# Optimization experiments

Hardware: AMD Instinct MI355X
Metric: run time of the kernel (lower is better)

## Reference

```python
import jax, jax.numpy as jnp
import numpy as np

S, B, D, H, F = 2048, 4, 1024, 2, 2048
HD = D // H  # head dim = 512
EPS = 1e-8   # forward() hardcodes 1e-8, ignoring init eps


def rmsnorm(x, w):
    ms = jnp.mean(x * x, axis=-1, keepdims=True)
    return w * (x / jnp.sqrt(ms + EPS))


def setup_inputs() -> dict:
    key = jax.random.key(0)
    ks = jax.random.split(key, 12)
    s = 0.02
    return {
        "x": jax.random.normal(ks[0], (S, B, D), jnp.float32),
        "w_norm1": 1.0 + s * jax.random.normal(ks[1], (D,), jnp.float32),
        "in_proj_w": s * jax.random.normal(ks[2], (3 * D, D), jnp.float32),
        "in_proj_b": s * jax.random.normal(ks[3], (3 * D,), jnp.float32),
        "out_proj_w": s * jax.random.normal(ks[4], (D, D), jnp.float32),
        "out_proj_b": s * jax.random.normal(ks[5], (D,), jnp.float32),
        "w_norm2": 1.0 + s * jax.random.normal(ks[6], (D,), jnp.float32),
        "W1": s * jax.random.normal(ks[7], (F, D), jnp.float32),
        "b1": s * jax.random.normal(ks[8], (F,), jnp.float32),
        "W2": s * jax.random.normal(ks[9], (D, F), jnp.float32),
        "b2": s * jax.random.normal(ks[10], (D,), jnp.float32),
    }


def reference(x, w_norm1, in_proj_w, in_proj_b, out_proj_w, out_proj_b,
              w_norm2, W1, b1, W2, b2):
    # pre-norm
    h = rmsnorm(x, w_norm1)                      # (S,B,D)
    # packed qkv projection (torch MultiheadAttention in_proj)
    qkv = h @ in_proj_w.T + in_proj_b            # (S,B,3D)
    q, k, v = jnp.split(qkv, 3, axis=-1)
    # (S,B,D) -> (B,H,S,HD)
    def heads(t):
        return t.reshape(S, B, H, HD).transpose(1, 2, 0, 3)
    q, k, v = heads(q), heads(k), heads(v)
    scores = jnp.einsum("bhsd,bhtd->bhst", q, k) / jnp.sqrt(jnp.float32(HD))
    causal = jnp.tril(jnp.ones((S, S), bool))
    scores = jnp.where(causal, scores, -jnp.inf)
    attn = jax.nn.softmax(scores, axis=-1)       # (B,H,S,S)
    ctx = jnp.einsum("bhst,bhtd->bhsd", attn, v)  # (B,H,S,HD)
    ctx = ctx.transpose(2, 0, 1, 3).reshape(S, B, D)
    attn_out = ctx @ out_proj_w.T + out_proj_b
    # residual 1
    x1 = x + attn_out
    # MLP: Linear -> exact GELU -> Linear
    m = rmsnorm(x1, w_norm2)
    mlp = jax.nn.gelu(m @ W1.T + b1, approximate=False) @ W2.T + b2
    return x1 + mlp
```

## Files before the change

### kernel.cpp

```cpp
#include <hip/hip_runtime.h>


typedef __bf16 bf16;
typedef bf16 bf16x8 __attribute__((ext_vector_type(8)));
typedef bf16 bf16x4 __attribute__((ext_vector_type(4)));
typedef float f32x4 __attribute__((ext_vector_type(4)));

#define MFMA16x16x32(A, B, C) __builtin_amdgcn_mfma_f32_16x16x32_bf16(A, B, C, 0, 0, 0)

__device__ __forceinline__ void gload16(const void* g, void* l) {
  __builtin_amdgcn_global_load_lds(
      (const __attribute__((address_space(1))) void*)g,
      (__attribute__((address_space(3))) void*)l, 16, 0, 0);
}

__global__ __launch_bounds__(256) void wcvt4(
    const float* __restrict__ s0, bf16* __restrict__ d0,
    const float* __restrict__ s1, bf16* __restrict__ d1,
    const float* __restrict__ s2, bf16* __restrict__ d2,
    const float* __restrict__ s3, bf16* __restrict__ d3)
{
  const int gid = blockIdx.x * 256 + threadIdx.x;
  const float* s; bf16* d; int off;
  if (gid < 786432)       { s = s0; d = d0; off = gid; }
  else if (gid < 1048576) { s = s1; d = d1; off = gid - 786432; }
  else if (gid < 1572864) { s = s2; d = d2; off = gid - 1048576; }
  else                    { s = s3; d = d3; off = gid - 1572864; }
  const int i = off * 4;
  const float4 v = *(const float4*)(s + i);
  bf16x4 o;
  o[0] = (bf16)v.x; o[1] = (bf16)v.y; o[2] = (bf16)v.z; o[3] = (bf16)v.w;
  *(bf16x4*)(d + i) = o;
}

__global__ __launch_bounds__(256) void rmsnorm_kernel(
    const float* __restrict__ x, const float* __restrict__ w, bf16* __restrict__ out)
{
  const int row = blockIdx.x;
  const int tid = threadIdx.x;
  const float4 v = *(const float4*)(x + (size_t)row * 1024 + tid * 4);
  float ss = v.x * v.x + v.y * v.y + v.z * v.z + v.w * v.w;
#pragma unroll
  for (int off = 1; off < 64; off <<= 1) ss += __shfl_xor(ss, off, 64);
  __shared__ float red[4];
  if ((tid & 63) == 0) red[tid >> 6] = ss;
  __syncthreads();
  const float tot = red[0] + red[1] + red[2] + red[3];
  const float inv = rsqrtf(tot * (1.0f / 1024.0f) + 1e-8f);
  const float4 g = *(const float4*)(w + tid * 4);
  bf16x4 o;
  o[0] = (bf16)(v.x * g.x * inv);
  o[1] = (bf16)(v.y * g.y * inv);
  o[2] = (bf16)(v.z * g.z * inv);
  o[3] = (bf16)(v.w * g.w * inv);
  *(bf16x4*)(out + (size_t)row * 1024 + tid * 4) = o;
}

enum { EPI_BF16 = 0, EPI_RES = 1, EPI_GELU = 2, EPI_QKV = 3 };

template <int EPI>
__global__ __launch_bounds__(256, 3) void gemm_bt2(
    const bf16* __restrict__ A,
    const bf16* __restrict__ B,
    const float* __restrict__ bias,
    const float* res,
    float* outF, bf16* outQ, bf16* outK, bf16* outV,
    int M, int N, int K)
{
  __shared__ bf16 lds[3 * 8192];
  const int tid = threadIdx.x;
  const int Nb = N >> 7;
  const int lin = blockIdx.x;
  const int sup = lin / (Nb << 4);
  const int rem = lin - sup * (Nb << 4);
  const int bm = (sup << 4) + (rem & 15);
  const int bn = rem >> 4;
  const int w = tid >> 6, lane = tid & 63;
  const int q = lane >> 4, lr = lane & 15;
  const int wr = (w >> 1) * 64, wc = (w & 1) * 64;
  f32x4 acc[4][4] = {};
  const int srow = lane >> 2;
  const int gch = ((lane & 3) - ((lane >> 3) & 3)) & 3;
  const bf16* Ab = A + (size_t)(bm * 128) * K;
  const bf16* Bb = B + (size_t)(bn * 128) * K;
  const int sw = ((q + (lr >> 1)) & 3) * 16;
  const int NK = K >> 5;

#define STAGE(dst, k0)                                                        \
  {                                                                           \
    bf16* De = (dst);                                                         \
    _Pragma("unroll")                                                         \
    for (int c = 0; c < 2; c++) {                                             \
      const int r = (w * 2 + c) * 16 + srow;                                  \
      gload16(Ab + (size_t)r * K + (k0) + gch * 8, De + (w * 2 + c) * 512);   \
      gload16(Bb + (size_t)r * K + (k0) + gch * 8, De + 4096 + (w * 2 + c) * 512); \
    }                                                                         \
  }

  bf16* rd = &lds[0];
  bf16* nx = &lds[8192];
  bf16* st = &lds[16384];
  STAGE(rd, 0);
  STAGE(nx, 32);
  asm volatile("s_waitcnt vmcnt(2)" ::: "memory");
  __builtin_amdgcn_s_barrier();
  asm volatile("" ::: "memory");

#pragma unroll 1
  for (int u = 0; u < NK; ++u) {
    if (u + 2 < NK) STAGE(st, (u + 2) * 32);
    const char* As = (const char*)rd;
    const char* Bs = (const char*)(rd + 4096);
    bf16x8 af[4], bfr[4];
#pragma unroll
    for (int mt = 0; mt < 4; mt++)
      af[mt] = *(const bf16x8*)(As + (wr + mt * 16 + lr) * 64 + sw);
#pragma unroll
    for (int nt = 0; nt < 4; nt++)
      bfr[nt] = *(const bf16x8*)(Bs + (wc + nt * 16 + lr) * 64 + sw);
#pragma unroll
    for (int mt = 0; mt < 4; mt++)
#pragma unroll
      for (int nt = 0; nt < 4; nt++)
        acc[mt][nt] = MFMA16x16x32(af[mt], bfr[nt], acc[mt][nt]);
    if (u + 1 < NK) {
      if (u + 2 < NK)
        asm volatile("s_waitcnt vmcnt(2) lgkmcnt(0)" ::: "memory");
      else
        asm volatile("s_waitcnt vmcnt(0) lgkmcnt(0)" ::: "memory");
      __builtin_amdgcn_s_barrier();
      asm volatile("" ::: "memory");
    }
    bf16* t = rd; rd = nx; nx = st; st = t;
  }
#undef STAGE

  const int gm0 = bm * 128 + wr + q * 4;
  const int gn0 = bn * 128 + wc + lr;
  bf16* outs = nullptr;
  if constexpr (EPI == EPI_QKV) {
    const int reg = (bn * 128) >> 10;
    outs = reg == 0 ? outQ : (reg == 1 ? outK : outV);
  } else {
    outs = outQ;
  }
#pragma unroll
  for (int nt = 0; nt < 4; nt++) {
    const int gn = gn0 + nt * 16;
    const float bv = bias[gn];
#pragma unroll
    for (int mt = 0; mt < 4; mt++) {
#pragma unroll
      for (int r = 0; r < 4; r++) {
        float v = acc[mt][nt][r] + bv;
        const int gm = gm0 + mt * 16 + r;
        if constexpr (EPI == EPI_GELU) {
          v = 0.5f * v * (1.0f + erff(v * 0.70710678118654752f));
          outs[(size_t)gm * N + gn] = (bf16)v;
        } else if constexpr (EPI == EPI_BF16) {
          outs[(size_t)gm * N + gn] = (bf16)v;
        } else if constexpr (EPI == EPI_QKV) {
          outs[(size_t)gm * 1024 + (gn & 1023)] = (bf16)v;
        } else {
          const size_t idx = (size_t)gm * N + gn;
          outF[idx] = v + res[idx];
        }
      }
    }
  }
}

__global__ __launch_bounds__(256) void vtrans_kernel(
    const bf16* __restrict__ vtmp, bf16* __restrict__ vt)
{
  __shared__ bf16 tile[64 * 72];
  const int kt = blockIdx.x;
  const int dt = blockIdx.y;
  const int bh = blockIdx.z;
  const int b = bh >> 1, h = bh & 1;
  const int tid = threadIdx.x;
#pragma unroll
  for (int it = 0; it < 2; it++) {
    const int key = it * 32 + (tid >> 3);
    const int dc = (tid & 7) * 8;
    const bf16x8 v = *(const bf16x8*)(vtmp +
        (size_t)((kt * 64 + key) * 4 + b) * 1024 + h * 512 + dt * 64 + dc);
    *(bf16x8*)&tile[key * 72 + dc] = v;
  }
  __syncthreads();
#pragma unroll
  for (int it = 0; it < 2; it++) {
    const int dim = it * 32 + (tid >> 3);
    const int kc = (tid & 7) * 8;
    bf16x8 o;
#pragma unroll
    for (int j = 0; j < 8; j++) o[j] = tile[(kc + j) * 72 + dim];
    *(bf16x8*)(vt + (size_t)bh * (1u << 20) +
               (size_t)(dt * 64 + dim) * 2048 + kt * 64 + kc) = o;
  }
}

__global__ __launch_bounds__(768, 3) void attn_kernel(
    const bf16* __restrict__ qb, const bf16* __restrict__ kb,
    const bf16* __restrict__ vtg, bf16* __restrict__ opart,
    float* __restrict__ lpart)
{
  __shared__ bf16 Ks[2][32 * 520];
  __shared__ bf16 Ps[2][4][16 * 40];
  const int bh = blockIdx.x;
  const int y = blockIdx.y;
  const int b = bh >> 1, h = bh & 1;
  const int tid = threadIdx.x;
  const int w = tid >> 6, lane = tid & 63;
  const int q = lane >> 4, lr = lane & 15;
  const float sc = 0.044194173824159216f;

  if (w < 4) {
    const bf16* krow0 = kb + (size_t)b * 1024 + h * 512 + lane * 8;
    for (int piece = 0; piece < 2; ++piece) {
      const int qt = piece ? (31 - y) : y;
      const int qrow0 = qt * 64;
      const int c0 = piece ? (qt + 1) : 0;
      const int c1 = c0 + qt + 1;
      bf16x8 Qf[16];
      {
        const bf16* qp = qb + (size_t)((qrow0 + w * 16 + lr) * 4 + b) * 1024 + h * 512 + q * 8;
#pragma unroll
        for (int kk = 0; kk < 16; kk++) Qf[kk] = *(const bf16x8*)(qp + kk * 32);
      }
#pragma unroll
      for (int j = 0; j < 8; j++)
        gload16(krow0 + (size_t)((c0 * 32 + w * 8 + j) * 4) * 1024,
                &Ks[c0 & 1][(w * 8 + j) * 520]);
      __syncthreads();
      const int myrow = qrow0 + w * 16 + q * 4;
      for (int t = c0; t <= c1; t++) {
        if (t < c1) {
          const int p = t & 1;
          const int kc = t * 32;
          if (t + 1 < c1) {
            const int kc2 = (t + 1) * 32;
#pragma unroll
            for (int j = 0; j < 8; j++)
              gload16(krow0 + (size_t)((kc2 + w * 8 + j) * 4) * 1024,
                      &Ks[1 - p][(w * 8 + j) * 520]);
          }
          const bool dead = kc > qrow0 + w * 16 + 15;
          float p0[4], p1[4];
          if (!dead) {
            f32x4 S0 = {}, S1 = {};
#pragma unroll
            for (int kk = 0; kk < 16; kk++) {
              const bf16x8 k0 = *(const bf16x8*)&Ks[p][lr * 520 + kk * 32 + q * 8];
              const bf16x8 k1 = *(const bf16x8*)&Ks[p][(16 + lr) * 520 + kk * 32 + q * 8];
              S0 = MFMA16x16x32(Qf[kk], k0, S0);
              S1 = MFMA16x16x32(Qf[kk], k1, S1);
            }
#pragma unroll
            for (int r = 0; r < 4; r++) {
              const int row = myrow + r;
              p0[r] = (kc + lr > row) ? 0.f : __expf(S0[r] * sc);
              p1[r] = (kc + 16 + lr > row) ? 0.f : __expf(S1[r] * sc);
            }
          } else {
#pragma unroll
            for (int r = 0; r < 4; r++) { p0[r] = 0.f; p1[r] = 0.f; }
          }
#pragma unroll
          for (int r = 0; r < 4; r++) {
            Ps[p][w][(q * 4 + r) * 40 + lr] = (bf16)p0[r];
            Ps[p][w][(q * 4 + r) * 40 + 16 + lr] = (bf16)p1[r];
          }
        }
        __syncthreads();
      }
    }
  } else {
    const int pw = w - 4;
    bf16x8 ones;
#pragma unroll
    for (int e = 0; e < 8; e++) ones[e] = (bf16)1.0f;
    const bf16* vbase = vtg + ((size_t)bh << 20) + (size_t)(pw * 64 + lr) * 2048 + q * 8;
    for (int piece = 0; piece < 2; ++piece) {
      const int qt = piece ? (31 - y) : y;
      const int qrow0 = qt * 64;
      const int c0 = piece ? (qt + 1) : 0;
      const int c1 = c0 + qt + 1;
      f32x4 O[4][4] = {};
      f32x4 lac = {};
      __syncthreads();
      for (int t = c0; t <= c1; t++) {
        if (t > c0) {
          const int p = (t - 1) & 1;
          const int kc = (t - 1) * 32;
          bf16x8 pa[4];
#pragma unroll
          for (int rt = 0; rt < 4; rt++)
            pa[rt] = *(const bf16x8*)&Ps[p][rt][lr * 40 + q * 8];
          if (pw < 4) {
            const bf16x8 psel = pw == 0 ? pa[0] : (pw == 1 ? pa[1] : (pw == 2 ? pa[2] : pa[3]));
            lac = MFMA16x16x32(psel, ones, lac);
          }
#pragma unroll
          for (int ct = 0; ct < 4; ct++) {
            const bf16x8 vf = *(const bf16x8*)(vbase + (size_t)(ct * 16) * 2048 + kc);
#pragma unroll
            for (int rt = 0; rt < 4; rt++)
              O[rt][ct] = MFMA16x16x32(pa[rt], vf, O[rt][ct]);
          }
        }
        __syncthreads();
      }
      bf16* op = opart + (size_t)piece * (8u << 20) + (size_t)bh * (1u << 20);
#pragma unroll
      for (int rt = 0; rt < 4; rt++)
#pragma unroll
        for (int ct = 0; ct < 4; ct++)
#pragma unroll
          for (int r = 0; r < 4; r++)
            op[(size_t)(qrow0 + rt * 16 + q * 4 + r) * 512 + pw * 64 + ct * 16 + lr] =
                (bf16)O[rt][ct][r];
      if (lr == 0 && pw < 4) {
#pragma unroll
        for (int r = 0; r < 4; r++)
          lpart[piece * 16384 + bh * 2048 + qrow0 + pw * 16 + q * 4 + r] = lac[r];
      }
    }
  }
}

__global__ __launch_bounds__(256) void attn_combine(
    const bf16* __restrict__ opart, const float* __restrict__ lpart,
    bf16* __restrict__ ctx)
{
  const int gid = blockIdx.x * 256 + threadIdx.x;
  const int bh = gid >> 17;
  const int rem = gid & 131071;
  const int row = rem >> 6;
  const int dc = (rem & 63) * 8;
  const size_t o = (size_t)bh * (1u << 20) + (size_t)row * 512 + dc;
  const bf16x8 a = *(const bf16x8*)(opart + o);
  const bf16x8 c = *(const bf16x8*)(opart + (size_t)(8u << 20) + o);
  const float inv = 1.0f /
      (lpart[bh * 2048 + row] + lpart[16384 + bh * 2048 + row]);
  bf16x8 ov;
#pragma unroll
  for (int e = 0; e < 8; e++) ov[e] = (bf16)(((float)a[e] + (float)c[e]) * inv);
  const int b = bh >> 1, h = bh & 1;
  *(bf16x8*)(ctx + (size_t)(row * 4 + b) * 1024 + h * 512 + dc) = ov;
}

extern "C" void kernel_launch(void* const* d_in, const int* in_sizes, int n_in,
                              void* d_out, int out_size, void* d_ws, size_t ws_size,
                              hipStream_t stream)
{
  (void)in_sizes; (void)n_in; (void)out_size; (void)ws_size;
  const float* x    = (const float*)d_in[0];
  const float* wn1  = (const float*)d_in[1];
  const float* wqkv = (const float*)d_in[2];
  const float* bqkv = (const float*)d_in[3];
  const float* wout = (const float*)d_in[4];
  const float* bout = (const float*)d_in[5];
  const float* wn2  = (const float*)d_in[6];
  const float* W1   = (const float*)d_in[7];
  const float* b1   = (const float*)d_in[8];
  const float* W2   = (const float*)d_in[9];
  const float* b2   = (const float*)d_in[10];
  float* out = (float*)d_out;

  char* ws = (char*)d_ws;
  const size_t Mi = 1u << 20;
  bf16* S0v = (bf16*)(ws);
  bf16* S1v = (bf16*)(ws + 16 * Mi);
  bf16* S2v = (bf16*)(ws + 32 * Mi);
  bf16* S3v = (bf16*)(ws + 48 * Mi);
  bf16* wqb = (bf16*)(ws + 64 * Mi);
  bf16* wob = (bf16*)(ws + 70 * Mi);
  bf16* w1b = (bf16*)(ws + 72 * Mi);
  bf16* w2b = (bf16*)(ws + 76 * Mi);
  const int M = 8192;

  wcvt4<<<8192, 256, 0, stream>>>(wqkv, wqb, wout, wob, W1, w1b, W2, w2b);
  rmsnorm_kernel<<<8192, 256, 0, stream>>>(x, wn1, S0v);
  gemm_bt2<EPI_QKV><<<64 * 24, 256, 0, stream>>>(
      S0v, wqb, bqkv, nullptr, nullptr, S1v, S2v, S3v, M, 3072, 1024);
  vtrans_kernel<<<dim3(32, 8, 8), 256, 0, stream>>>(S3v, S0v);
  attn_kernel<<<dim3(8, 32), 768, 0, stream>>>(
      S1v, S2v, S0v, (bf16*)d_out, (float*)S3v);
  attn_combine<<<4096, 256, 0, stream>>>((const bf16*)d_out, (const float*)S3v, S1v);
  gemm_bt2<EPI_RES><<<64 * 8, 256, 0, stream>>>(
      S1v, wob, bout, x, out, nullptr, nullptr, nullptr, M, 1024, 1024);
  rmsnorm_kernel<<<8192, 256, 0, stream>>>(out, wn2, S0v);
  gemm_bt2<EPI_GELU><<<64 * 16, 256, 0, stream>>>(
      S0v, w1b, b1, nullptr, nullptr, S2v, nullptr, nullptr, M, 2048, 1024);
  gemm_bt2<EPI_RES><<<64 * 8, 256, 0, stream>>>(
      S2v, w2b, b2, out, out, nullptr, nullptr, nullptr, M, 1024, 2048);
}
```

Baseline: 420.4 us.

## Use double-buffered LDS in GEMM and raise wave priority around attention MFMAs

The GEMM main loop drops from a three-stage LDS ring with hand-tuned vmcnt waits to a two-buffer scheme that prefetches one tile ahead and ends each iteration with __syncthreads. This cuts LDS use from 48KB to 32KB per block, which may allow more resident blocks. The cost is shallower prefetch and a full wait on outstanding loads at each barrier. Separately, the attention score MFMA loop is wrapped in s_setprio(1)/s_setprio(0) so waves issuing matrix work get scheduling priority.

Measured after the change: 428.0 us. No clear change (+1.8%).

```diff
diff --git a/kernel.cpp b/kernel.cpp
--- a/kernel.cpp
+++ b/kernel.cpp
@@ -67,7 +67,7 @@
     float* outF, bf16* outQ, bf16* outK, bf16* outV,
     int M, int N, int K)
 {
-  __shared__ bf16 lds[3 * 8192];
+  __shared__ bf16 lds[2][8192];
   const int tid = threadIdx.x;
   const int Nb = N >> 7;
   const int lin = blockIdx.x;
@@ -97,20 +97,15 @@
     }                                                                         \
   }
 
-  bf16* rd = &lds[0];
-  bf16* nx = &lds[8192];
-  bf16* st = &lds[16384];
-  STAGE(rd, 0);
-  STAGE(nx, 32);
-  asm volatile("s_waitcnt vmcnt(2)" ::: "memory");
-  __builtin_amdgcn_s_barrier();
-  asm volatile("" ::: "memory");
-
+  STAGE(&lds[0][0], 0);
+  __syncthreads();
 #pragma unroll 1
   for (int u = 0; u < NK; ++u) {
-    if (u + 2 < NK) STAGE(st, (u + 2) * 32);
-    const char* As = (const char*)rd;
-    const char* Bs = (const char*)(rd + 4096);
+    bf16* cur = &lds[u & 1][0];
+    bf16* nxt = &lds[(u + 1) & 1][0];
+    if (u + 1 < NK) STAGE(nxt, (u + 1) * 32);
+    const char* As = (const char*)cur;
+    const char* Bs = (const char*)(cur + 4096);
     bf16x8 af[4], bfr[4];
 #pragma unroll
     for (int mt = 0; mt < 4; mt++)
@@ -123,15 +118,7 @@
 #pragma unroll
       for (int nt = 0; nt < 4; nt++)
         acc[mt][nt] = MFMA16x16x32(af[mt], bfr[nt], acc[mt][nt]);
-    if (u + 1 < NK) {
-      if (u + 2 < NK)
-        asm volatile("s_waitcnt vmcnt(2) lgkmcnt(0)" ::: "memory");
-      else
-        asm volatile("s_waitcnt vmcnt(0) lgkmcnt(0)" ::: "memory");
-      __builtin_amdgcn_s_barrier();
-      asm volatile("" ::: "memory");
-    }
-    bf16* t = rd; rd = nx; nx = st; st = t;
+    __syncthreads();
   }
 #undef STAGE
 
@@ -249,6 +236,7 @@
           float p0[4], p1[4];
           if (!dead) {
             f32x4 S0 = {}, S1 = {};
+            __builtin_amdgcn_s_setprio(1);
 #pragma unroll
             for (int kk = 0; kk < 16; kk++) {
               const bf16x8 k0 = *(const bf16x8*)&Ks[p][lr * 520 + kk * 32 + q * 8];
@@ -256,6 +244,7 @@
               S0 = MFMA16x16x32(Qf[kk], k0, S0);
               S1 = MFMA16x16x32(Qf[kk], k1, S1);
             }
+            __builtin_amdgcn_s_setprio(0);
 #pragma unroll
             for (int r = 0; r < 4; r++) {
               const int row = myrow + r;
```
